# Optimization experiments

Hardware: AMD Instinct MI355X
Metric: run time of the kernel (lower is better)

The kernel has to match this reference:

```python
import jax, jax.numpy as jnp
import numpy as np

N_HEADS = 2
WINDOW = 4
BLOCK = 256


def _get_rel_emb(emb, length):
    # emb: [1, 2*WINDOW+1, K] -> [1, 2*length-1, K]
    pad = max(length - (WINDOW + 1), 0)
    start = max((WINDOW + 1) - length, 0)
    e = jnp.pad(emb, ((0, 0), (pad, pad), (0, 0)))
    return e[:, start:start + 2 * length - 1]


def _rel_to_abs(x):
    # x: [b, h, l, 2l-1] -> [b, h, l, l] (skew trick)
    b, h, l, _ = x.shape
    x = jnp.pad(x, ((0, 0), (0, 0), (0, 0), (0, 1))).reshape(b, h, 2 * l * l)
    x = jnp.pad(x, ((0, 0), (0, 0), (0, l - 1))).reshape(b, h, l + 1, 2 * l - 1)
    return x[:, :, :l, l - 1:]


def _abs_to_rel(x):
    # x: [b, h, l, l] -> [b, h, l, 2l-1] (inverse skew)
    b, h, l, _ = x.shape
    x = jnp.pad(x, ((0, 0), (0, 0), (0, 0), (0, l - 1))).reshape(b, h, l * (2 * l - 1))
    x = jnp.pad(x, ((0, 0), (0, 0), (l, 0))).reshape(b, h, l, 2 * l)
    return x[:, :, :, 1:]


def _attention(x, c, attn_mask, Wq, bq, Wk, bk, Wv, bv, Wo, bo, emb_rel_k, emb_rel_v):
    B, C, T = x.shape
    H, K = N_HEADS, C // N_HEADS
    # projections (torch Linear on [B,T,C])
    q = (jnp.einsum('bct,cd->btd', x, Wq) + bq).reshape(B, T, H, K).transpose(0, 2, 1, 3)
    k = (jnp.einsum('bct,cd->btd', c, Wk) + bk).reshape(B, T, H, K).transpose(0, 2, 1, 3)
    v = (jnp.einsum('bct,cd->btd', c, Wv) + bv).reshape(B, T, H, K).transpose(0, 2, 1, 3)
    qs = q / jnp.sqrt(jnp.float32(K))
    scores = jnp.einsum('bhtk,bhsk->bhts', qs, k)  # [B,H,T,T]
    # relative-position key logits (heads_share=True -> single table)
    rel_k = _get_rel_emb(emb_rel_k, T)[0]          # [2T-1, K]
    rel_logits = jnp.einsum('bhtk,rk->bhtr', qs, rel_k)
    scores = scores + _rel_to_abs(rel_logits)
    # proximal bias: -log1p(|i-j|)
    r = jnp.arange(T, dtype=jnp.float32)
    scores = scores - jnp.log1p(jnp.abs(r[:, None] - r[None, :]))[None, None]
    # attn mask + block-local mask (block mask active because mask is given)
    ij = jnp.arange(T)
    block_ok = jnp.abs(ij[:, None] - ij[None, :]) <= BLOCK
    valid = (attn_mask != 0) & block_ok[None, None]
    scores = jnp.where(valid, scores, jnp.float32(-1e4))
    p = jax.nn.softmax(scores, axis=-1)
    out = jnp.einsum('bhts,bhsk->bhtk', p, v)
    # relative-position value contribution
    rel_v = _get_rel_emb(emb_rel_v, T)[0]          # [2T-1, K]
    out = out + jnp.einsum('bhtr,rk->bhtk', _abs_to_rel(p), rel_v)
    out = out.transpose(0, 2, 1, 3).reshape(B, T, C)
    y = jnp.einsum('btd,do->bto', out, Wo) + bo
    return y.transpose(0, 2, 1)  # [B, out_channels, T]


def setup_inputs() -> dict:
    key = jax.random.key(0)
    ks = jax.random.split(key, 8)
    B, C, T = 4, 192, 2048
    K = C // N_HEADS
    s = jnp.float32(0.05)
    rel_std = jnp.float32(K ** -0.5)
    return {
        'x': jax.random.normal(ks[0], (B, C, T), jnp.float32),
        'c': jax.random.normal(ks[1], (B, C, T), jnp.float32),
        'Wq': jax.random.normal(ks[2], (C, C), jnp.float32) * s,
        'bq': jnp.zeros((C,), jnp.float32),
        'Wk': jax.random.normal(ks[3], (C, C), jnp.float32) * s,
        'bk': jnp.zeros((C,), jnp.float32),
        'Wv': jax.random.normal(ks[4], (C, C), jnp.float32) * s,
        'bv': jnp.zeros((C,), jnp.float32),
        'Wo': jax.random.normal(ks[5], (C, C), jnp.float32) * s,
        'bo': jnp.zeros((C,), jnp.float32),
        'emb_rel_k': jax.random.normal(ks[6], (1, 2 * WINDOW + 1, K), jnp.float32) * rel_std,
        'emb_rel_v': jax.random.normal(ks[7], (1, 2 * WINDOW + 1, K), jnp.float32) * rel_std,
        'attn_mask': jnp.ones((B, 1, T, T), jnp.int32),
    }


def reference(x, c, Wq, bq, Wk, bk, Wv, bv, Wo, bo, emb_rel_k, emb_rel_v, attn_mask):
    return _attention(x, c, attn_mask, Wq, bq, Wk, bk, Wv, bv, Wo, bo, emb_rel_k, emb_rel_v)
```

## Files before the change

kernel.cpp:

```cpp
#include <hip/hip_runtime.h>
#include <hip/hip_bf16.h>

#define B_DIM 4
#define C_DIM 192
#define T_SEQ 2048
#define H_DIM 2
#define K_DIM 96
#define BAND 256
#define IT 16
#define NJT 34
#define WSLOT 544
#define WPD 556
#define PRS (2*WPD)
#define PMW 17
#define XSTR 200
#define PDS 40

typedef __attribute__((ext_vector_type(8))) short bf16x8;
typedef __attribute__((ext_vector_type(4))) short bf16x4;
typedef __attribute__((ext_vector_type(4))) float f32x4;
#define MFMA16 __builtin_amdgcn_mfma_f32_16x16x32_bf16

__device__ __forceinline__ short f2bf_bits(float f) {
    union { __hip_bfloat16 h; short s; } u; u.h = __float2bfloat16(f); return u.s;
}

#define OFF_WT(m)  ((size_t)(m)*73728)
#define OFF_BQS    ((size_t)294912)
#define OFF_RELKBF ((size_t)295680)
#define OFF_RVT    ((size_t)298752)
#define OFF_QBF    ((size_t)304896)
#define OFF_KBF    (OFF_QBF + 3145728)
#define OFF_VTB    (OFF_KBF + 3145728)
#define OFF_OBTC   (OFF_VTB + 3145728)

__global__ __launch_bounds__(256)
void prep_kernel(const float* __restrict__ Wq, const float* __restrict__ Wk,
                 const float* __restrict__ Wv, const float* __restrict__ Wo,
                 const float* __restrict__ bq, const float* __restrict__ relk,
                 const float* __restrict__ relv, char* __restrict__ ws)
{
    const float qscale = 0.10206207261596577f;
    const int bidx = blockIdx.x;
    const int tid  = threadIdx.x;

    if (bidx < 144) {
        __shared__ float tile[32][33];
        const int mi = bidx / 36, tl = bidx % 36;
        const int R0 = (tl / 6) * 32, C0 = (tl % 6) * 32;
        const float* src = (mi == 0) ? Wq : (mi == 1) ? Wk : (mi == 2) ? Wv : Wo;
        const int r = tid >> 5, cc = tid & 31;
        #pragma unroll
        for (int i = 0; i < 4; ++i) {
            const int rr = r + 8*i;
            tile[rr][cc] = src[(R0 + rr)*C_DIM + C0 + cc];
        }
        __syncthreads();
        short* dst = (short*)(ws + OFF_WT(mi));
        #pragma unroll
        for (int i = 0; i < 4; ++i) {
            const int rr = r + 8*i;
            float v = tile[cc][rr];
            if (mi == 0) v *= qscale;
            dst[(C0 + rr)*C_DIM + R0 + cc] = f2bf_bits(v);
        }
        return;
    }
    if (tid < C_DIM)
        ((float*)(ws + OFF_BQS))[tid] = bq[tid]*qscale;
    short* rkb = (short*)(ws + OFF_RELKBF);
    for (int idx = tid; idx < 16*K_DIM; idx += 256) {
        const int row = idx / K_DIM;
        rkb[idx] = (row < 9) ? f2bf_bits(relk[idx]) : (short)0;
    }
    short* rvt = (short*)(ws + OFF_RVT);
    for (int idx = tid; idx < K_DIM*32; idx += 256) {
        const int col = idx >> 5, dd = idx & 31;
        rvt[idx] = (dd < 9) ? f2bf_bits(relv[dd*K_DIM + col]) : (short)0;
    }
}

__global__ __launch_bounds__(256, 6)
void proj_kernel(const float* __restrict__ x, const float* __restrict__ cin,
                 const float* __restrict__ bk, const float* __restrict__ bv,
                 char* __restrict__ ws)
{
    __shared__ short sb[IT*XSTR];
    const int hw = blockIdx.x;
    const int L  = (hw & 7)*192 + (hw >> 3);
    const int which = L % 3;
    const int rest  = L / 3;
    const int b  = rest >> 7;
    const int t0 = (rest & 127) * IT;
    const int tid = threadIdx.x;
    const int wave = tid >> 6, lane = tid & 63;
    const int q4 = lane >> 4, lr = lane & 15;

    const float* src = (which == 0) ? x : cin;
    for (int l = tid; l < 768; l += 256) {
        const int cr = l >> 2, u = l & 3;
        const float4 v4 = *reinterpret_cast<const float4*>(
            src + (size_t)(b*C_DIM + cr)*T_SEQ + t0 + 4*u);
        sb[(4*u+0)*XSTR + cr] = f2bf_bits(v4.x);
        sb[(4*u+1)*XSTR + cr] = f2bf_bits(v4.y);
        sb[(4*u+2)*XSTR + cr] = f2bf_bits(v4.z);
        sb[(4*u+3)*XSTR + cr] = f2bf_bits(v4.w);
    }
    __syncthreads();

    const short* WT = (const short*)(ws + OFF_WT(which));
    f32x4 a[3];
    #pragma unroll
    for (int j = 0; j < 3; ++j) a[j] = (f32x4){0.f,0.f,0.f,0.f};
    for (int kc = 0; kc < 6; ++kc) {
        const int ko = kc*32 + q4*8;
        const bf16x8 sf = *reinterpret_cast<const bf16x8*>(sb + lr*XSTR + ko);
        #pragma unroll
        for (int j = 0; j < 3; ++j) {
            const bf16x8 wf = *reinterpret_cast<const bf16x8*>(
                WT + ((3*wave + j)*16 + lr)*C_DIM + ko);
            a[j] = (which == 2) ? MFMA16(wf, sf, a[j], 0, 0, 0)
                                : MFMA16(sf, wf, a[j], 0, 0, 0);
        }
    }

    const float* bqs = (const float*)(ws + OFF_BQS);
    #pragma unroll
    for (int j = 0; j < 3; ++j) {
        const int dt = 3*wave + j;
        if (which <= 1) {
            const int d = dt*16 + lr, h = d/K_DIM, kk = d%K_DIM;
            const int bh = b*H_DIM + h;
            const float bias = (which == 0) ? bqs[d] : bk[d];
            short* dst = (short*)(ws + (which == 0 ? OFF_QBF : OFF_KBF));
            #pragma unroll
            for (int e = 0; e < 4; ++e) {
                const int t = t0 + q4*4 + e;
                dst[((size_t)bh*T_SEQ + t)*K_DIM + kk] = f2bf_bits(a[j][e] + bias);
            }
        } else {
            short* vtb = (short*)(ws + OFF_VTB);
            #pragma unroll
            for (int e = 0; e < 4; ++e) {
                const int d = dt*16 + q4*4 + e, h = d/K_DIM, kk = d%K_DIM;
                const int bh = b*H_DIM + h;
                vtb[((size_t)bh*K_DIM + kk)*T_SEQ + t0 + lr] = f2bf_bits(a[j][e] + bv[d]);
            }
        }
    }
}

__global__ __launch_bounds__(256, 4)
void attn_kernel(const int* __restrict__ mask, char* __restrict__ ws)
{
    __shared__ __align__(16) float ps[IT*WPD];
    __shared__ float lt[257];
    __shared__ __align__(16) char upool[1664];
    unsigned* pm_s = (unsigned*)upool;
    float*    rl   = (float*)(upool + 1088);
    short*    pd_s = (short*)upool;

    const short* qbf = (const short*)(ws + OFF_QBF);
    const short* kbf = (const short*)(ws + OFF_KBF);
    const short* vtb = (const short*)(ws + OFF_VTB);
    const short* rkb = (const short*)(ws + OFF_RELKBF);
    const short* rvt = (const short*)(ws + OFF_RVT);
    short* obtc = (short*)(ws + OFF_OBTC);

    const int L    = ((blockIdx.x & 7) << 7) + (blockIdx.x >> 3);
    const int b    = L >> 8;
    const int rem  = L & 255;
    const int i0   = (rem >> 1) * IT;
    const int head = rem & 1;
    const int tid = threadIdx.x;
    const int wave = tid >> 6, lane = tid & 63;
    const int q4 = lane >> 4, lr = lane & 15;

    const int jlo  = max(0, i0 - BAND);
    const int jhi  = min(T_SEQ - 1, i0 + IT - 1 + BAND);
    const int wlen = jhi - jlo + 1;
    const size_t qk_base = (size_t)(b*H_DIM + head) * T_SEQ * K_DIM;

    bf16x8 qa[3];
    {
        const short* qrow = qbf + qk_base + (size_t)(i0 + lr)*K_DIM + q4*8;
        #pragma unroll
        for (int kc = 0; kc < 3; ++kc)
            qa[kc] = *reinterpret_cast<const bf16x8*>(qrow + kc*32);
    }

    for (int idx = tid; idx < 257; idx += 256) lt[idx] = log1pf((float)idx);

    for (int idx = tid; idx < IT*PMW; idx += 256) {
        const int r = idx / PMW, w = idx % PMW;
        const int* mrow = mask + ((size_t)b*T_SEQ + i0 + r)*T_SEQ;
        unsigned bits = 0;
        #pragma unroll
        for (int g4 = 0; g4 < 8; ++g4) {
            const int jg = jlo + 32*w + 4*g4;
            if (jg + 3 < T_SEQ) {
                const int4 mv = *reinterpret_cast<const int4*>(mrow + jg);
                bits |= (unsigned)(mv.x != 0) << (4*g4);
                bits |= (unsigned)(mv.y != 0) << (4*g4+1);
                bits |= (unsigned)(mv.z != 0) << (4*g4+2);
                bits |= (unsigned)(mv.w != 0) << (4*g4+3);
            } else {
                #pragma unroll
                for (int e = 0; e < 4; ++e)
                    if (jg + e < T_SEQ && mrow[jg+e] != 0) bits |= 1u << (4*g4+e);
            }
        }
        pm_s[idx] = bits;
    }

    {
        int jt = wave;
        int jr = jlo + jt*16 + lr; if (jr > T_SEQ-1) jr = T_SEQ-1;
        const short* kr = kbf + qk_base + (size_t)jr*K_DIM + q4*8;
        bf16x8 kf0 = *reinterpret_cast<const bf16x8*>(kr);
        bf16x8 kf1 = *reinterpret_cast<const bf16x8*>(kr + 32);
        bf16x8 kf2 = *reinterpret_cast<const bf16x8*>(kr + 64);
        while (true) {
            const int jn = jt + 4;
            const bool more = (jn < NJT);
            bf16x8 nf0, nf1, nf2;
            if (more) {
                int jr2 = jlo + jn*16 + lr; if (jr2 > T_SEQ-1) jr2 = T_SEQ-1;
                const short* kr2 = kbf + qk_base + (size_t)jr2*K_DIM + q4*8;
                nf0 = *reinterpret_cast<const bf16x8*>(kr2);
                nf1 = *reinterpret_cast<const bf16x8*>(kr2 + 32);
                nf2 = *reinterpret_cast<const bf16x8*>(kr2 + 64);
            }
            f32x4 s = {0.f,0.f,0.f,0.f};
            s = MFMA16(qa[0], kf0, s, 0, 0, 0);
            s = MFMA16(qa[1], kf1, s, 0, 0, 0);
            s = MFMA16(qa[2], kf2, s, 0, 0, 0);
            float* pr = ps + (q4*4)*WPD + jt*16 + lr;
            pr[0*WPD] = s[0]; pr[1*WPD] = s[1]; pr[2*WPD] = s[2]; pr[3*WPD] = s[3];
            if (!more) break;
            kf0 = nf0; kf1 = nf1; kf2 = nf2;
            jt = jn;
        }
    }
    if (wave == 3) {
        const short* krow = rkb + lr*K_DIM + q4*8;
        f32x4 rs = {0.f,0.f,0.f,0.f};
        #pragma unroll
        for (int kc = 0; kc < 3; ++kc)
            rs = MFMA16(qa[kc], *reinterpret_cast<const bf16x8*>(krow + kc*32), rs, 0, 0, 0);
        if (lr < 9) {
            #pragma unroll
            for (int e = 0; e < 4; ++e)
                rl[(q4*4 + e)*9 + lr] = rs[e];
        }
    }
    __syncthreads();

    {
        const int r = tid >> 4, sj = tid & 15;
        const int i = i0 + r;
        float* prow = ps + r*WPD;
        float vals[36];
        float m = -INFINITY;
        #pragma unroll
        for (int mm = 0; mm < 9; ++mm) {
            const int j0 = 4*sj + 64*mm;
            float4 pv = make_float4(0.f,0.f,0.f,0.f);
            unsigned mb = 0;
            if (j0 < WSLOT) {
                pv = *reinterpret_cast<const float4*>(prow + j0);
                mb = pm_s[r*PMW + (j0 >> 5)] >> (j0 & 31);
            }
            const float pe[4] = {pv.x, pv.y, pv.z, pv.w};
            #pragma unroll
            for (int e = 0; e < 4; ++e) {
                const int j = j0 + e;
                float val = -INFINITY;
                if (j0 < WSLOT && j < wlen) {
                    const int jg = jlo + j, dd = jg - i;
                    const int ad = dd < 0 ? -dd : dd;
                    if (ad <= BAND && ((mb >> e) & 1)) {
                        val = pe[e] - lt[ad];
                        if ((unsigned)(dd + 4) <= 8u) val += rl[r*9 + dd + 4];
                    }
                }
                vals[mm*4 + e] = val;
                m = fmaxf(m, val);
            }
        }
        #pragma unroll
        for (int off = 8; off > 0; off >>= 1) m = fmaxf(m, __shfl_xor(m, off, 64));
        if (m == -INFINITY) m = 0.f;
        float ssum = 0.f;
        #pragma unroll
        for (int u = 0; u < 36; ++u) { vals[u] = __expf(vals[u] - m); ssum += vals[u]; }
        #pragma unroll
        for (int off = 8; off > 0; off >>= 1) ssum += __shfl_xor(ssum, off, 64);
        const float inv = ssum > 0.f ? 1.f/ssum : 0.f;
        short* pbrow = (short*)prow;
        #pragma unroll
        for (int mm = 0; mm < 9; ++mm) {
            const int j0 = 4*sj + 64*mm;
            if (j0 < WSLOT) {
                bf16x4 w;
                #pragma unroll
                for (int e = 0; e < 4; ++e) w[e] = f2bf_bits(vals[mm*4+e]*inv);
                *reinterpret_cast<bf16x4*>(pbrow + j0) = w;
            }
        }
    }
    __syncthreads();

    for (int idx = tid; idx < IT*PDS; idx += 256) {
        const int r = idx / PDS, kk = idx % PDS;
        short v = 0;
        if (kk < 9) {
            const int jg = i0 + r + kk - 4;
            if (jg >= 0 && jg < T_SEQ)
                v = ((const short*)ps)[r*PRS + (jg - jlo)];
        }
        pd_s[idx] = v;
    }

    const short* pbh = (const short*)ps;
    f32x4 o0 = {0.f,0.f,0.f,0.f}, o1 = {0.f,0.f,0.f,0.f};
    {
        const short* vbase0 = vtb + qk_base + (size_t)(wave*16 + lr)*T_SEQ;
        const short* vbase1 = vtb + qk_base + (size_t)((wave+4)*16 + lr)*T_SEQ;
        int tc = jlo + q4*8; if (tc > T_SEQ-8) tc = T_SEQ-8;
        bf16x8 vb0 = *reinterpret_cast<const bf16x8*>(vbase0 + tc);
        bf16x8 vb1 = {};
        if (wave < 2) vb1 = *reinterpret_cast<const bf16x8*>(vbase1 + tc);
        for (int kc = 0; kc < NJT/2; ++kc) {
            bf16x8 nv0, nv1;
            const bool more = (kc + 1 < NJT/2);
            if (more) {
                int tn = jlo + (kc+1)*32 + q4*8; if (tn > T_SEQ-8) tn = T_SEQ-8;
                nv0 = *reinterpret_cast<const bf16x8*>(vbase0 + tn);
                if (wave < 2) nv1 = *reinterpret_cast<const bf16x8*>(vbase1 + tn);
            }
            const bf16x8 pa = *reinterpret_cast<const bf16x8*>(pbh + lr*PRS + kc*32 + q4*8);
            o0 = MFMA16(pa, vb0, o0, 0, 0, 0);
            if (wave < 2) o1 = MFMA16(pa, vb1, o1, 0, 0, 0);
            if (more) { vb0 = nv0; if (wave < 2) vb1 = nv1; }
        }
    }
    __syncthreads();

    {
        const bf16x8 pda = *reinterpret_cast<const bf16x8*>(pd_s + lr*PDS + q4*8);
        const bf16x8 rv0 = *reinterpret_cast<const bf16x8*>(rvt + (wave*16 + lr)*32 + q4*8);
        o0 = MFMA16(pda, rv0, o0, 0, 0, 0);
        if (wave < 2) {
            const bf16x8 rv1 = *reinterpret_cast<const bf16x8*>(rvt + ((wave+4)*16 + lr)*32 + q4*8);
            o1 = MFMA16(pda, rv1, o1, 0, 0, 0);
        }
    }
    #pragma unroll
    for (int u = 0; u < 2; ++u) {
        if (u == 1 && wave >= 2) break;
        const int nt = u ? wave + 4 : wave;
        const f32x4 oc = u ? o1 : o0;
        const int col = head*K_DIM + nt*16 + lr;
        #pragma unroll
        for (int e = 0; e < 4; ++e) {
            const int i = i0 + q4*4 + e;
            obtc[((size_t)b*T_SEQ + i)*C_DIM + col] = f2bf_bits(oc[e]);
        }
    }
}

__global__ __launch_bounds__(256)
void oproj_kernel(const float* __restrict__ bo, float* __restrict__ y,
                  const char* __restrict__ ws)
{
    const int bid = ((blockIdx.x & 7) << 6) + (blockIdx.x >> 3);
    const int b   = bid >> 7;
    const int t0  = (bid & 127) * 16;
    const int tid = threadIdx.x;
    const int wave = tid >> 6, lane = tid & 63;
    const int q4 = lane >> 4, lr = lane & 15;

    const short* WoT  = (const short*)(ws + OFF_WT(3));
    const short* obtc = (const short*)(ws + OFF_OBTC);

    f32x4 a[3];
    #pragma unroll
    for (int j = 0; j < 3; ++j) a[j] = (f32x4){0.f,0.f,0.f,0.f};
    for (int kc = 0; kc < 6; ++kc) {
        const int ko = kc*32 + q4*8;
        const bf16x8 bf = *reinterpret_cast<const bf16x8*>(
            obtc + ((size_t)b*T_SEQ + t0 + lr)*C_DIM + ko);
        #pragma unroll
        for (int j = 0; j < 3; ++j) {
            const bf16x8 af = *reinterpret_cast<const bf16x8*>(
                WoT + ((3*wave + j)*16 + lr)*C_DIM + ko);
            a[j] = MFMA16(af, bf, a[j], 0, 0, 0);
        }
    }
    #pragma unroll
    for (int j = 0; j < 3; ++j) {
        #pragma unroll
        for (int e = 0; e < 4; ++e) {
            const int d = (3*wave + j)*16 + q4*4 + e;
            y[((size_t)b*C_DIM + d)*T_SEQ + t0 + lr] = a[j][e] + bo[d];
        }
    }
}

extern "C" void kernel_launch(void* const* d_in, const int* in_sizes, int n_in,
                              void* d_out, int out_size, void* d_ws, size_t ws_size,
                              hipStream_t stream)
{
    const float* x    = (const float*)d_in[0];
    const float* c    = (const float*)d_in[1];
    const float* Wq   = (const float*)d_in[2];
    const float* bq   = (const float*)d_in[3];
    const float* Wk   = (const float*)d_in[4];
    const float* bk   = (const float*)d_in[5];
    const float* Wv   = (const float*)d_in[6];
    const float* bv   = (const float*)d_in[7];
    const float* Wo   = (const float*)d_in[8];
    const float* bo   = (const float*)d_in[9];
    const float* relk = (const float*)d_in[10];
    const float* relv = (const float*)d_in[11];
    const int*   mask = (const int*)d_in[12];
    float*       y    = (float*)d_out;
    char*        ws   = (char*)d_ws;

    hipLaunchKernelGGL(prep_kernel, dim3(145), dim3(256), 0, stream,
                       Wq, Wk, Wv, Wo, bq, relk, relv, ws);
    hipLaunchKernelGGL(proj_kernel, dim3(B_DIM*(T_SEQ/16)*3), dim3(256), 0, stream,
                       x, c, bk, bv, ws);
    hipLaunchKernelGGL(attn_kernel, dim3(B_DIM*H_DIM*(T_SEQ/IT)), dim3(256), 0, stream,
                       mask, ws);
    hipLaunchKernelGGL(oproj_kernel, dim3(B_DIM*(T_SEQ/16)), dim3(256), 0, stream,
                       bo, y, ws);
}
```

Before: 183.9 us.

## Double query tile to 32 rows, use 1024-thread attention blocks, read mask directly

Raises the query tile from 16 to 32 rows. Attention blocks grow to 16 waves that split the score tiles and the PV tiles, and the staged bitmask is replaced by direct int4 mask loads during softmax. The softmax moves to base-2 exp with log2 scaling folded into the q scale and the log table. Projection and output-projection kernels each compute two 16-row tiles per block so weight loads are reused. The aim is less redundant K/V band loading per query row and fewer blocks; the cost is larger blocks with lower occupancy and the loss of the previous K/V prefetch pipelining.

```diff
diff --git a/kernel.cpp b/kernel.cpp
--- a/kernel.cpp
+++ b/kernel.cpp
@@ -7,12 +7,11 @@
 #define H_DIM 2
 #define K_DIM 96
 #define BAND 256
-#define IT 16
+#define IT 32
 #define NJT 34
 #define WSLOT 544
 #define WPD 556
 #define PRS (2*WPD)
-#define PMW 17
 #define XSTR 200
 #define PDS 40
 
@@ -40,7 +39,7 @@
                  const float* __restrict__ bq, const float* __restrict__ relk,
                  const float* __restrict__ relv, char* __restrict__ ws)
 {
-    const float qscale = 0.10206207261596577f;
+    const float qscale = 0.14724445972f;
     const int bidx = blockIdx.x;
     const int tid  = threadIdx.x;
 
@@ -80,25 +79,25 @@
     }
 }
 
-__global__ __launch_bounds__(256, 6)
+__global__ __launch_bounds__(256)
 void proj_kernel(const float* __restrict__ x, const float* __restrict__ cin,
                  const float* __restrict__ bk, const float* __restrict__ bv,
                  char* __restrict__ ws)
 {
-    __shared__ short sb[IT*XSTR];
+    __shared__ short sb[2*IT*XSTR/2];
     const int hw = blockIdx.x;
-    const int L  = (hw & 7)*192 + (hw >> 3);
+    const int L  = (hw & 7)*96 + (hw >> 3);
     const int which = L % 3;
     const int rest  = L / 3;
-    const int b  = rest >> 7;
-    const int t0 = (rest & 127) * IT;
+    const int b  = rest >> 6;
+    const int t0 = (rest & 63) * 32;
     const int tid = threadIdx.x;
     const int wave = tid >> 6, lane = tid & 63;
     const int q4 = lane >> 4, lr = lane & 15;
 
     const float* src = (which == 0) ? x : cin;
-    for (int l = tid; l < 768; l += 256) {
-        const int cr = l >> 2, u = l & 3;
+    for (int l = tid; l < 1536; l += 256) {
+        const int cr = l >> 3, u = l & 7;
         const float4 v4 = *reinterpret_cast<const float4*>(
             src + (size_t)(b*C_DIM + cr)*T_SEQ + t0 + 4*u);
         sb[(4*u+0)*XSTR + cr] = f2bf_bits(v4.x);
@@ -109,18 +108,27 @@
     __syncthreads();
 
     const short* WT = (const short*)(ws + OFF_WT(which));
-    f32x4 a[3];
+    f32x4 a[3][2];
     #pragma unroll
-    for (int j = 0; j < 3; ++j) a[j] = (f32x4){0.f,0.f,0.f,0.f};
+    for (int j = 0; j < 3; ++j) {
+        a[j][0] = (f32x4){0.f,0.f,0.f,0.f};
+        a[j][1] = (f32x4){0.f,0.f,0.f,0.f};
+    }
     for (int kc = 0; kc < 6; ++kc) {
         const int ko = kc*32 + q4*8;
-        const bf16x8 sf = *reinterpret_cast<const bf16x8*>(sb + lr*XSTR + ko);
+        const bf16x8 sf0 = *reinterpret_cast<const bf16x8*>(sb + lr*XSTR + ko);
+        const bf16x8 sf1 = *reinterpret_cast<const bf16x8*>(sb + (16 + lr)*XSTR + ko);
         #pragma unroll
         for (int j = 0; j < 3; ++j) {
             const bf16x8 wf = *reinterpret_cast<const bf16x8*>(
                 WT + ((3*wave + j)*16 + lr)*C_DIM + ko);
-            a[j] = (which == 2) ? MFMA16(wf, sf, a[j], 0, 0, 0)
-                                : MFMA16(sf, wf, a[j], 0, 0, 0);
+            if (which == 2) {
+                a[j][0] = MFMA16(wf, sf0, a[j][0], 0, 0, 0);
+                a[j][1] = MFMA16(wf, sf1, a[j][1], 0, 0, 0);
+            } else {
+                a[j][0] = MFMA16(sf0, wf, a[j][0], 0, 0, 0);
+                a[j][1] = MFMA16(sf1, wf, a[j][1], 0, 0, 0);
+            }
         }
     }
 
@@ -134,31 +142,35 @@
             const float bias = (which == 0) ? bqs[d] : bk[d];
             short* dst = (short*)(ws + (which == 0 ? OFF_QBF : OFF_KBF));
             #pragma unroll
-            for (int e = 0; e < 4; ++e) {
-                const int t = t0 + q4*4 + e;
-                dst[((size_t)bh*T_SEQ + t)*K_DIM + kk] = f2bf_bits(a[j][e] + bias);
-            }
+            for (int rt = 0; rt < 2; ++rt)
+                #pragma unroll
+                for (int e = 0; e < 4; ++e) {
+                    const int t = t0 + rt*16 + q4*4 + e;
+                    dst[((size_t)bh*T_SEQ + t)*K_DIM + kk] = f2bf_bits(a[j][rt][e] + bias);
+                }
         } else {
             short* vtb = (short*)(ws + OFF_VTB);
             #pragma unroll
-            for (int e = 0; e < 4; ++e) {
-                const int d = dt*16 + q4*4 + e, h = d/K_DIM, kk = d%K_DIM;
-                const int bh = b*H_DIM + h;
-                vtb[((size_t)bh*K_DIM + kk)*T_SEQ + t0 + lr] = f2bf_bits(a[j][e] + bv[d]);
-            }
-        }
-    }
-}
-
-__global__ __launch_bounds__(256, 4)
+            for (int rt = 0; rt < 2; ++rt)
+                #pragma unroll
+                for (int e = 0; e < 4; ++e) {
+                    const int d = dt*16 + q4*4 + e, h = d/K_DIM, kk = d%K_DIM;
+                    const int bh = b*H_DIM + h;
+                    vtb[((size_t)bh*K_DIM + kk)*T_SEQ + t0 + rt*16 + lr] =
+                        f2bf_bits(a[j][rt][e] + bv[d]);
+                }
+        }
+    }
+}
+
+__global__ __launch_bounds__(1024, 8)
 void attn_kernel(const int* __restrict__ mask, char* __restrict__ ws)
 {
     __shared__ __align__(16) float ps[IT*WPD];
     __shared__ float lt[257];
-    __shared__ __align__(16) char upool[1664];
-    unsigned* pm_s = (unsigned*)upool;
-    float*    rl   = (float*)(upool + 1088);
-    short*    pd_s = (short*)upool;
+    __shared__ __align__(16) char upool[2560];
+    float* rl   = (float*)upool;
+    short* pd_s = (short*)upool;
 
     const short* qbf = (const short*)(ws + OFF_QBF);
     const short* kbf = (const short*)(ws + OFF_KBF);
@@ -167,82 +179,43 @@
     const short* rvt = (const short*)(ws + OFF_RVT);
     short* obtc = (short*)(ws + OFF_OBTC);
 
-    const int L    = ((blockIdx.x & 7) << 7) + (blockIdx.x >> 3);
-    const int b    = L >> 8;
-    const int rem  = L & 255;
+    const int L    = ((blockIdx.x & 7) << 6) + (blockIdx.x >> 3);
+    const int b    = L >> 7;
+    const int rem  = L & 127;
     const int i0   = (rem >> 1) * IT;
     const int head = rem & 1;
-    const int tid = threadIdx.x;
+    const int tid  = threadIdx.x;
     const int wave = tid >> 6, lane = tid & 63;
     const int q4 = lane >> 4, lr = lane & 15;
+    const int ri = wave & 1, wg = wave >> 1;
 
     const int jlo  = max(0, i0 - BAND);
     const int jhi  = min(T_SEQ - 1, i0 + IT - 1 + BAND);
     const int wlen = jhi - jlo + 1;
     const size_t qk_base = (size_t)(b*H_DIM + head) * T_SEQ * K_DIM;
 
+    for (int idx = tid; idx < 257; idx += 1024) lt[idx] = log2f((float)(1 + idx));
+
     bf16x8 qa[3];
     {
-        const short* qrow = qbf + qk_base + (size_t)(i0 + lr)*K_DIM + q4*8;
+        const short* qrow = qbf + qk_base + (size_t)(i0 + ri*16 + lr)*K_DIM + q4*8;
         #pragma unroll
         for (int kc = 0; kc < 3; ++kc)
             qa[kc] = *reinterpret_cast<const bf16x8*>(qrow + kc*32);
     }
 
-    for (int idx = tid; idx < 257; idx += 256) lt[idx] = log1pf((float)idx);
-
-    for (int idx = tid; idx < IT*PMW; idx += 256) {
-        const int r = idx / PMW, w = idx % PMW;
-        const int* mrow = mask + ((size_t)b*T_SEQ + i0 + r)*T_SEQ;
-        unsigned bits = 0;
-        #pragma unroll
-        for (int g4 = 0; g4 < 8; ++g4) {
-            const int jg = jlo + 32*w + 4*g4;
-            if (jg + 3 < T_SEQ) {
-                const int4 mv = *reinterpret_cast<const int4*>(mrow + jg);
-                bits |= (unsigned)(mv.x != 0) << (4*g4);
-                bits |= (unsigned)(mv.y != 0) << (4*g4+1);
-                bits |= (unsigned)(mv.z != 0) << (4*g4+2);
-                bits |= (unsigned)(mv.w != 0) << (4*g4+3);
-            } else {
-                #pragma unroll
-                for (int e = 0; e < 4; ++e)
-                    if (jg + e < T_SEQ && mrow[jg+e] != 0) bits |= 1u << (4*g4+e);
-            }
-        }
-        pm_s[idx] = bits;
-    }
-
-    {
-        int jt = wave;
-        int jr = jlo + jt*16 + lr; if (jr > T_SEQ-1) jr = T_SEQ-1;
-        const short* kr = kbf + qk_base + (size_t)jr*K_DIM + q4*8;
-        bf16x8 kf0 = *reinterpret_cast<const bf16x8*>(kr);
-        bf16x8 kf1 = *reinterpret_cast<const bf16x8*>(kr + 32);
-        bf16x8 kf2 = *reinterpret_cast<const bf16x8*>(kr + 64);
-        while (true) {
-            const int jn = jt + 4;
-            const bool more = (jn < NJT);
-            bf16x8 nf0, nf1, nf2;
-            if (more) {
-                int jr2 = jlo + jn*16 + lr; if (jr2 > T_SEQ-1) jr2 = T_SEQ-1;
-                const short* kr2 = kbf + qk_base + (size_t)jr2*K_DIM + q4*8;
-                nf0 = *reinterpret_cast<const bf16x8*>(kr2);
-                nf1 = *reinterpret_cast<const bf16x8*>(kr2 + 32);
-                nf2 = *reinterpret_cast<const bf16x8*>(kr2 + 64);
-            }
-            f32x4 s = {0.f,0.f,0.f,0.f};
-            s = MFMA16(qa[0], kf0, s, 0, 0, 0);
-            s = MFMA16(qa[1], kf1, s, 0, 0, 0);
-            s = MFMA16(qa[2], kf2, s, 0, 0, 0);
-            float* pr = ps + (q4*4)*WPD + jt*16 + lr;
-            pr[0*WPD] = s[0]; pr[1*WPD] = s[1]; pr[2*WPD] = s[2]; pr[3*WPD] = s[3];
-            if (!more) break;
-            kf0 = nf0; kf1 = nf1; kf2 = nf2;
-            jt = jn;
-        }
-    }
-    if (wave == 3) {
+    for (int jt = wg; jt < NJT; jt += 8) {
+        int jr = jlo + jt*16 + lr;
+        if (jr > T_SEQ-1) jr = T_SEQ-1;
+        const short* krow = kbf + qk_base + (size_t)jr*K_DIM + q4*8;
+        f32x4 s = {0.f,0.f,0.f,0.f};
+        #pragma unroll
+        for (int kc = 0; kc < 3; ++kc)
+            s = MFMA16(qa[kc], *reinterpret_cast<const bf16x8*>(krow + kc*32), s, 0, 0, 0);
+        float* pr = ps + (ri*16 + q4*4)*WPD + jt*16 + lr;
+        pr[0*WPD] = s[0]; pr[1*WPD] = s[1]; pr[2*WPD] = s[2]; pr[3*WPD] = s[3];
+    }
+    if (wg == 7) {
         const short* krow = rkb + lr*K_DIM + q4*8;
         f32x4 rs = {0.f,0.f,0.f,0.f};
         #pragma unroll
@@ -251,35 +224,37 @@
         if (lr < 9) {
             #pragma unroll
             for (int e = 0; e < 4; ++e)
-                rl[(q4*4 + e)*9 + lr] = rs[e];
+                rl[(ri*16 + q4*4 + e)*9 + lr] = rs[e];
         }
     }
     __syncthreads();
 
     {
-        const int r = tid >> 4, sj = tid & 15;
+        const int r = tid >> 5, sj = tid & 31;
         const int i = i0 + r;
+        const int* mrow = mask + ((size_t)b*T_SEQ + i)*T_SEQ;
         float* prow = ps + r*WPD;
-        float vals[36];
+        float vals[20];
         float m = -INFINITY;
         #pragma unroll
-        for (int mm = 0; mm < 9; ++mm) {
-            const int j0 = 4*sj + 64*mm;
+        for (int mm = 0; mm < 5; ++mm) {
+            const int j0 = 4*sj + 128*mm;
             float4 pv = make_float4(0.f,0.f,0.f,0.f);
-            unsigned mb = 0;
-            if (j0 < WSLOT) {
+            int4 mv = make_int4(0,0,0,0);
+            if (j0 < wlen) {
                 pv = *reinterpret_cast<const float4*>(prow + j0);
-                mb = pm_s[r*PMW + (j0 >> 5)] >> (j0 & 31);
+                mv = *reinterpret_cast<const int4*>(mrow + jlo + j0);
             }
             const float pe[4] = {pv.x, pv.y, pv.z, pv.w};
+            const int me[4] = {mv.x, mv.y, mv.z, mv.w};
             #pragma unroll
             for (int e = 0; e < 4; ++e) {
                 const int j = j0 + e;
                 float val = -INFINITY;
-                if (j0 < WSLOT && j < wlen) {
-                    const int jg = jlo + j, dd = jg - i;
+                if (j0 < wlen && j < wlen) {
+                    const int dd = jlo + j - i;
                     const int ad = dd < 0 ? -dd : dd;
-                    if (ad <= BAND && ((mb >> e) & 1)) {
+                    if (ad <= BAND && me[e] != 0) {
                         val = pe[e] - lt[ad];
                         if ((unsigned)(dd + 4) <= 8u) val += rl[r*9 + dd + 4];
                     }
@@ -289,18 +264,18 @@
             }
         }
         #pragma unroll
-        for (int off = 8; off > 0; off >>= 1) m = fmaxf(m, __shfl_xor(m, off, 64));
+        for (int off = 16; off > 0; off >>= 1) m = fmaxf(m, __shfl_xor(m, off, 64));
         if (m == -INFINITY) m = 0.f;
         float ssum = 0.f;
         #pragma unroll
-        for (int u = 0; u < 36; ++u) { vals[u] = __expf(vals[u] - m); ssum += vals[u]; }
-        #pragma unroll
-        for (int off = 8; off > 0; off >>= 1) ssum += __shfl_xor(ssum, off, 64);
+        for (int u = 0; u < 20; ++u) { vals[u] = exp2f(vals[u] - m); ssum += vals[u]; }
+        #pragma unroll
+        for (int off = 16; off > 0; off >>= 1) ssum += __shfl_xor(ssum, off, 64);
         const float inv = ssum > 0.f ? 1.f/ssum : 0.f;
         short* pbrow = (short*)prow;
         #pragma unroll
-        for (int mm = 0; mm < 9; ++mm) {
-            const int j0 = 4*sj + 64*mm;
+        for (int mm = 0; mm < 5; ++mm) {
+            const int j0 = 4*sj + 128*mm;
             if (j0 < WSLOT) {
                 bf16x4 w;
                 #pragma unroll
@@ -311,7 +286,7 @@
     }
     __syncthreads();
 
-    for (int idx = tid; idx < IT*PDS; idx += 256) {
+    for (int idx = tid; idx < IT*PDS; idx += 1024) {
         const int r = idx / PDS, kk = idx % PDS;
         short v = 0;
         if (kk < 9) {
@@ -322,50 +297,31 @@
         pd_s[idx] = v;
     }
 
-    const short* pbh = (const short*)ps;
-    f32x4 o0 = {0.f,0.f,0.f,0.f}, o1 = {0.f,0.f,0.f,0.f};
-    {
-        const short* vbase0 = vtb + qk_base + (size_t)(wave*16 + lr)*T_SEQ;
-        const short* vbase1 = vtb + qk_base + (size_t)((wave+4)*16 + lr)*T_SEQ;
-        int tc = jlo + q4*8; if (tc > T_SEQ-8) tc = T_SEQ-8;
-        bf16x8 vb0 = *reinterpret_cast<const bf16x8*>(vbase0 + tc);
-        bf16x8 vb1 = {};
-        if (wave < 2) vb1 = *reinterpret_cast<const bf16x8*>(vbase1 + tc);
+    f32x4 o = {0.f,0.f,0.f,0.f};
+    const int pri = wave & 1, pnt = wave >> 1;
+    if (wave < 12) {
+        const short* pbh = (const short*)ps;
+        const short* vbase = vtb + qk_base + (size_t)(pnt*16 + lr)*T_SEQ;
         for (int kc = 0; kc < NJT/2; ++kc) {
-            bf16x8 nv0, nv1;
-            const bool more = (kc + 1 < NJT/2);
-            if (more) {
-                int tn = jlo + (kc+1)*32 + q4*8; if (tn > T_SEQ-8) tn = T_SEQ-8;
-                nv0 = *reinterpret_cast<const bf16x8*>(vbase0 + tn);
-                if (wave < 2) nv1 = *reinterpret_cast<const bf16x8*>(vbase1 + tn);
-            }
-            const bf16x8 pa = *reinterpret_cast<const bf16x8*>(pbh + lr*PRS + kc*32 + q4*8);
-            o0 = MFMA16(pa, vb0, o0, 0, 0, 0);
-            if (wave < 2) o1 = MFMA16(pa, vb1, o1, 0, 0, 0);
-            if (more) { vb0 = nv0; if (wave < 2) vb1 = nv1; }
+            const bf16x8 pa = *reinterpret_cast<const bf16x8*>(
+                pbh + (pri*16 + lr)*PRS + kc*32 + q4*8);
+            int tc = jlo + kc*32 + q4*8;
+            if (tc > T_SEQ-8) tc = T_SEQ-8;
+            const bf16x8 vb = *reinterpret_cast<const bf16x8*>(vbase + tc);
+            o = MFMA16(pa, vb, o, 0, 0, 0);
         }
     }
     __syncthreads();
 
-    {
-        const bf16x8 pda = *reinterpret_cast<const bf16x8*>(pd_s + lr*PDS + q4*8);
-        const bf16x8 rv0 = *reinterpret_cast<const bf16x8*>(rvt + (wave*16 + lr)*32 + q4*8);
-        o0 = MFMA16(pda, rv0, o0, 0, 0, 0);
-        if (wave < 2) {
-            const bf16x8 rv1 = *reinterpret_cast<const bf16x8*>(rvt + ((wave+4)*16 + lr)*32 + q4*8);
-            o1 = MFMA16(pda, rv1, o1, 0, 0, 0);
-        }
-    }
-    #pragma unroll
-    for (int u = 0; u < 2; ++u) {
-        if (u == 1 && wave >= 2) break;
-        const int nt = u ? wave + 4 : wave;
-        const f32x4 oc = u ? o1 : o0;
-        const int col = head*K_DIM + nt*16 + lr;
+    if (wave < 12) {
+        const bf16x8 pda = *reinterpret_cast<const bf16x8*>(pd_s + (pri*16 + lr)*PDS + q4*8);
+        const bf16x8 rv  = *reinterpret_cast<const bf16x8*>(rvt + (pnt*16 + lr)*32 + q4*8);
+        o = MFMA16(pda, rv, o, 0, 0, 0);
+        const int col = head*K_DIM + pnt*16 + lr;
         #pragma unroll
         for (int e = 0; e < 4; ++e) {
-            const int i = i0 + q4*4 + e;
-            obtc[((size_t)b*T_SEQ + i)*C_DIM + col] = f2bf_bits(oc[e]);
+            const int i = i0 + pri*16 + q4*4 + e;
+            obtc[((size_t)b*T_SEQ + i)*C_DIM + col] = f2bf_bits(o[e]);
         }
     }
 }
@@ -374,9 +330,9 @@
 void oproj_kernel(const float* __restrict__ bo, float* __restrict__ y,
                   const char* __restrict__ ws)
 {
-    const int bid = ((blockIdx.x & 7) << 6) + (blockIdx.x >> 3);
-    const int b   = bid >> 7;
-    const int t0  = (bid & 127) * 16;
+    const int bid = ((blockIdx.x & 7) << 5) + (blockIdx.x >> 3);
+    const int b   = bid >> 6;
+    const int t0  = (bid & 63) * 32;
     const int tid = threadIdx.x;
     const int wave = tid >> 6, lane = tid & 63;
     const int q4 = lane >> 4, lr = lane & 15;
@@ -384,27 +340,35 @@
     const short* WoT  = (const short*)(ws + OFF_WT(3));
     const short* obtc = (const short*)(ws + OFF_OBTC);
 
-    f32x4 a[3];
+    f32x4 a[3][2];
     #pragma unroll
-    for (int j = 0; j < 3; ++j) a[j] = (f32x4){0.f,0.f,0.f,0.f};
+    for (int j = 0; j < 3; ++j) {
+        a[j][0] = (f32x4){0.f,0.f,0.f,0.f};
+        a[j][1] = (f32x4){0.f,0.f,0.f,0.f};
+    }
     for (int kc = 0; kc < 6; ++kc) {
         const int ko = kc*32 + q4*8;
-        const bf16x8 bf = *reinterpret_cast<const bf16x8*>(
+        const bf16x8 bf0 = *reinterpret_cast<const bf16x8*>(
             obtc + ((size_t)b*T_SEQ + t0 + lr)*C_DIM + ko);
+        const bf16x8 bf1 = *reinterpret_cast<const bf16x8*>(
+            obtc + ((size_t)b*T_SEQ + t0 + 16 + lr)*C_DIM + ko);
         #pragma unroll
         for (int j = 0; j < 3; ++j) {
             const bf16x8 af = *reinterpret_cast<const bf16x8*>(
                 WoT + ((3*wave + j)*16 + lr)*C_DIM + ko);
-            a[j] = MFMA16(af, bf, a[j], 0, 0, 0);
+            a[j][0] = MFMA16(af, bf0, a[j][0], 0, 0, 0);
+            a[j][1] = MFMA16(af, bf1, a[j][1], 0, 0, 0);
         }
     }
     #pragma unroll
     for (int j = 0; j < 3; ++j) {
         #pragma unroll
-        for (int e = 0; e < 4; ++e) {
-            const int d = (3*wave + j)*16 + q4*4 + e;
-            y[((size_t)b*C_DIM + d)*T_SEQ + t0 + lr] = a[j][e] + bo[d];
-        }
+        for (int rt = 0; rt < 2; ++rt)
+            #pragma unroll
+            for (int e = 0; e < 4; ++e) {
+                const int d = (3*wave + j)*16 + q4*4 + e;
+                y[((size_t)b*C_DIM + d)*T_SEQ + t0 + rt*16 + lr] = a[j][rt][e] + bo[d];
+            }
     }
 }
 
@@ -430,10 +394,10 @@
 
     hipLaunchKernelGGL(prep_kernel, dim3(145), dim3(256), 0, stream,
                        Wq, Wk, Wv, Wo, bq, relk, relv, ws);
-    hipLaunchKernelGGL(proj_kernel, dim3(B_DIM*(T_SEQ/16)*3), dim3(256), 0, stream,
+    hipLaunchKernelGGL(proj_kernel, dim3(B_DIM*(T_SEQ/32)*3), dim3(256), 0, stream,
                        x, c, bk, bv, ws);
-    hipLaunchKernelGGL(attn_kernel, dim3(B_DIM*H_DIM*(T_SEQ/IT)), dim3(256), 0, stream,
+    hipLaunchKernelGGL(attn_kernel, dim3(B_DIM*H_DIM*(T_SEQ/IT)), dim3(1024), 0, stream,
                        mask, ws);
-    hipLaunchKernelGGL(oproj_kernel, dim3(B_DIM*(T_SEQ/16)), dim3(256), 0, stream,
+    hipLaunchKernelGGL(oproj_kernel, dim3(B_DIM*(T_SEQ/32)), dim3(256), 0, stream,
                        bo, y, ws);
 }
```

Result: faster. 167.9 us (-8.7%).
